# Kernel tuning notes

Hardware: AMD Instinct MI355X
Metric: run time of the kernel (lower is better)

Reference implementation:

```python
import jax, jax.numpy as jnp
import numpy as np

S = 64            # out_size
EXPAND = 1.25
FEAT_DOWN = 8
DEG2RAD = np.pi / 180.0


def setup_inputs() -> dict:
    key = jax.random.key(0)
    k1, k2, k3 = jax.random.split(key, 3)
    B, C, Hf, Wf = 2, 64, 128, 128
    N = 256
    feat = jax.random.normal(k1, (B, C, Hf, Wf), dtype=jnp.float32)
    r = jax.random.uniform(k2, (N, 5), dtype=jnp.float32)
    # values chosen so the (buggy-but-faithful) normalized-coordinate affine
    # actually samples inside the feature map (see shape_source note)
    cx = (r[:, 0] - 0.5) * 10.0
    cy = (r[:, 1] - 0.5) * 10.0
    w = 50.0 + 350.0 * r[:, 2]
    h = 50.0 + 350.0 * r[:, 3]
    deg = (r[:, 4] - 0.5) * 180.0
    obb = jnp.stack([cx, cy, w, h, deg], axis=1)
    bix = jax.random.randint(k3, (N,), 0, B)
    return {"feat": feat, "obb": obb, "bix": bix}


def _grids(obb):
    """Replicates obb_to_affine + F.affine_grid(align_corners=False).
    Returns normalized grid coords gx, gy of shape (N, S, S)."""
    scale = 1.0 / FEAT_DOWN
    cx = obb[:, 0] * scale
    cy = obb[:, 1] * scale
    ws = obb[:, 2] * scale * EXPAND
    hs = obb[:, 3] * scale * EXPAND
    th = obb[:, 4] * DEG2RAD
    c = jnp.cos(th)
    s_ = jnp.sin(th)
    sx = ws / S
    sy = hs / S
    # faithful to source: M = [[c*sx, -sin*sy, cx], [expand*sx, c*sy, cy]]
    m00 = c * sx
    m01 = -s_ * sy
    m02 = cx
    m10 = EXPAND * sx   # source uses `s` = expand here, NOT sin(theta)
    m11 = c * sy
    m12 = cy
    # affine_grid base coords (align_corners=False): (2k+1)/S - 1
    base = (2.0 * jnp.arange(S, dtype=obb.dtype) + 1.0) / S - 1.0
    x = base[None, None, :]   # output column -> x
    y = base[None, :, None]   # output row    -> y
    gx = m00[:, None, None] * x + m01[:, None, None] * y + m02[:, None, None]
    gy = m10[:, None, None] * x + m11[:, None, None] * y + m12[:, None, None]
    return gx, gy


def _rotated_roi_pool(feat, obb, bix):
    B, C, Hf, Wf = feat.shape
    gx, gy = _grids(obb)                       # (N,S,S)
    # grid_sample unnormalize (align_corners=False)
    ix = ((gx + 1.0) * Wf - 1.0) * 0.5
    iy = ((gy + 1.0) * Hf - 1.0) * 0.5
    x0f = jnp.floor(ix)
    y0f = jnp.floor(iy)
    wx1 = ix - x0f
    wy1 = iy - y0f
    x0 = x0f.astype(jnp.int32)
    y0 = y0f.astype(jnp.int32)
    b = bix[:, None, None].astype(jnp.int32)   # (N,1,1)

    def corner(yi, xi):
        valid = (xi >= 0) & (xi < Wf) & (yi >= 0) & (yi < Hf)
        yc = jnp.clip(yi, 0, Hf - 1)
        xc = jnp.clip(xi, 0, Wf - 1)
        v = feat[b, :, yc, xc]                 # (N,S,S,C) gather
        return v * valid[..., None].astype(feat.dtype)

    out = (corner(y0, x0)         * ((1.0 - wy1) * (1.0 - wx1))[..., None]
         + corner(y0, x0 + 1)     * ((1.0 - wy1) * wx1)[..., None]
         + corner(y0 + 1, x0)     * (wy1 * (1.0 - wx1))[..., None]
         + corner(y0 + 1, x0 + 1) * (wy1 * wx1)[..., None])
    return jnp.transpose(out, (0, 3, 1, 2))    # (N,C,S,S)


def reference(feat, obb, bix):
    return _rotated_roi_pool(feat, obb, bix)
```

## Files before the change

kernel.cpp:

```cpp
#include <hip/hip_runtime.h>
#include <math.h>

#define S 64
#define NC 64
#define HF 128
#define WF 128
#define HW (HF * WF)
#define SS (S * S)
#define EXPANDF 1.25f
#define FEAT_DOWN_INV 0.125f
#define DEG2RADF 0.017453292519943295f

__device__ __forceinline__ unsigned int f32_to_bf16_rne(float v) {
    unsigned int u = __float_as_uint(v);
    return (u + 0x7FFFu + ((u >> 16) & 1u)) >> 16;
}
__device__ __forceinline__ float bf16_bits_to_f32(unsigned int h) {
    return __uint_as_float(h << 16);
}

__global__ __launch_bounds__(256) void nchw_to_nhwc_bf16_kernel(
    const float*    __restrict__ feat,
    unsigned short* __restrict__ featT)
{
    __shared__ float lds[64 * 65];
    const int bh  = blockIdx.x;
    const int b   = bh >> 7;
    const int h   = bh & (HF - 1);
    const int w0  = blockIdx.y << 6;
    const int tid = threadIdx.x;
    const int t4  = tid >> 6;
    const int t64 = tid & 63;

#pragma unroll
    for (int k = 0; k < 16; ++k) {
        const int c = (k << 2) + t4;
        lds[t64 * 65 + c] = feat[(((size_t)b * NC + c) * HF + h) * WF + w0 + t64];
    }
    __syncthreads();
#pragma unroll
    for (int k = 0; k < 16; ++k) {
        const int w = (k << 2) + t4;
        featT[(((size_t)b * HF + h) * WF + w0 + w) * NC + t64] =
            (unsigned short)f32_to_bf16_rne(lds[w * 65 + t64]);
    }
}

__global__ __launch_bounds__(256) void RotatedROIPool_kernel(
    const unsigned short* __restrict__ featT,
    const float*          __restrict__ obb,
    const int*            __restrict__ bix,
    float*                __restrict__ out,
    int nwg_per_xcd)
{
    __shared__ float lds[64 * 65];

    const int bid = blockIdx.x;
    const int wg  = (bid & 7) * nwg_per_xcd + (bid >> 3);
    const int n   = wg >> 6;
    const int i   = wg & 63;

    const int tid  = threadIdx.x;
    const int wv   = tid >> 6;
    const int lane = tid & 63;
    const int s    = lane >> 3;
    const int c8   = lane & 7;

    const float o0 = obb[n * 5 + 0];
    const float o1 = obb[n * 5 + 1];
    const float o2 = obb[n * 5 + 2];
    const float o3 = obb[n * 5 + 3];
    const float o4 = obb[n * 5 + 4];

    const float cx  = o0 * FEAT_DOWN_INV;
    const float cy  = o1 * FEAT_DOWN_INV;
    const float wsc = o2 * FEAT_DOWN_INV * EXPANDF;
    const float hsc = o3 * FEAT_DOWN_INV * EXPANDF;
    const float th  = o4 * DEG2RADF;

    float sth, cth;
    sincosf(th, &sth, &cth);

    const float sx  = wsc * (1.0f / (float)S);
    const float sy  = hsc * (1.0f / (float)S);
    const float m00 = cth * sx;
    const float m01 = -sth * sy;
    const float m10 = EXPANDF * sx;
    const float m11 = cth * sy;

    const float yg = (2.0f * (float)i + 1.0f) * (1.0f / (float)S) - 1.0f;
    const float hx = m01 * yg + cx;
    const float hy = m11 * yg + cy;

    const int b = bix[n];
    const unsigned char* __restrict__ pb =
        (const unsigned char*)featT + (size_t)b * ((size_t)HW * NC * 2);

#pragma unroll
    for (int sg = 0; sg < 2; ++sg) {
        const int j = (wv << 4) + (sg << 3) + s;

        const float xg = (2.0f * (float)j + 1.0f) * (1.0f / (float)S) - 1.0f;
        const float gx = m00 * xg + hx;
        const float gy = m10 * xg + hy;

        const float ix = ((gx + 1.0f) * (float)WF - 1.0f) * 0.5f;
        const float iy = ((gy + 1.0f) * (float)HF - 1.0f) * 0.5f;

        const float x0f = floorf(ix);
        const float y0f = floorf(iy);
        const float wx1 = ix - x0f;
        const float wy1 = iy - y0f;
        const float wx0 = 1.0f - wx1;
        const float wy0 = 1.0f - wy1;

        const int x0 = (int)x0f;
        const int y0 = (int)y0f;
        const int x1 = x0 + 1;
        const int y1 = y0 + 1;

        const float vx0 = (x0 >= 0 && x0 < WF) ? 1.0f : 0.0f;
        const float vx1 = (x1 >= 0 && x1 < WF) ? 1.0f : 0.0f;
        const float vy0 = (y0 >= 0 && y0 < HF) ? 1.0f : 0.0f;
        const float vy1 = (y1 >= 0 && y1 < HF) ? 1.0f : 0.0f;

        const float w00 = wy0 * wx0 * vy0 * vx0;
        const float w01 = wy0 * wx1 * vy0 * vx1;
        const float w10 = wy1 * wx0 * vy1 * vx0;
        const float w11 = wy1 * wx1 * vy1 * vx1;

        const int x0c = min(max(x0, 0), WF - 1);
        const int x1c = min(max(x1, 0), WF - 1);
        const int y0c = min(max(y0, 0), HF - 1);
        const int y1c = min(max(y1, 0), HF - 1);

        const uint4 a00 = *((const uint4*)(pb + ((size_t)(y0c * WF + x0c) << 7)) + c8);
        const uint4 a01 = *((const uint4*)(pb + ((size_t)(y0c * WF + x1c) << 7)) + c8);
        const uint4 a10 = *((const uint4*)(pb + ((size_t)(y1c * WF + x0c) << 7)) + c8);
        const uint4 a11 = *((const uint4*)(pb + ((size_t)(y1c * WF + x1c) << 7)) + c8);

        const unsigned int* u00 = (const unsigned int*)&a00;
        const unsigned int* u01 = (const unsigned int*)&a01;
        const unsigned int* u10 = (const unsigned int*)&a10;
        const unsigned int* u11 = (const unsigned int*)&a11;

        float* L = lds + j * 65 + (c8 << 3);
#pragma unroll
        for (int m = 0; m < 4; ++m) {
            const float f00l = bf16_bits_to_f32(u00[m] & 0xFFFFu);
            const float f01l = bf16_bits_to_f32(u01[m] & 0xFFFFu);
            const float f10l = bf16_bits_to_f32(u10[m] & 0xFFFFu);
            const float f11l = bf16_bits_to_f32(u11[m] & 0xFFFFu);
            const float f00h = bf16_bits_to_f32(u00[m] >> 16);
            const float f01h = bf16_bits_to_f32(u01[m] >> 16);
            const float f10h = bf16_bits_to_f32(u10[m] >> 16);
            const float f11h = bf16_bits_to_f32(u11[m] >> 16);
            L[2 * m + 0] = w00 * f00l + w01 * f01l + w10 * f10l + w11 * f11l;
            L[2 * m + 1] = w00 * f00h + w01 * f01h + w10 * f10h + w11 * f11h;
        }
    }

    __syncthreads();

    float* __restrict__ ob = out + (size_t)n * NC * SS + (size_t)i * S;
    const int jg = tid & 15;
    const int cl = tid >> 4;
#pragma unroll
    for (int k = 0; k < 4; ++k) {
        const int c = (k << 4) + cl;
        float4 t;
        t.x = lds[(jg * 4 + 0) * 65 + c];
        t.y = lds[(jg * 4 + 1) * 65 + c];
        t.z = lds[(jg * 4 + 2) * 65 + c];
        t.w = lds[(jg * 4 + 3) * 65 + c];
        *(float4*)(ob + (size_t)c * SS + (jg << 2)) = t;
    }
}

__global__ __launch_bounds__(256) void RotatedROIPool_nchw_kernel(
    const float* __restrict__ feat, const float* __restrict__ obb,
    const int* __restrict__ bix, float* __restrict__ out)
{
    const int tid = threadIdx.x, pid = blockIdx.x;
    const int n = pid >> 4, patch = pid & 15;
    const int pi = (patch >> 2) << 4, pj = (patch & 3) << 4;
    const int w = tid >> 6, lane = tid & 63;
    const int i = pi + ((w >> 1) << 3) + (lane >> 3);
    const int j = pj + ((w & 1) << 3) + (lane & 7);
    const int c0 = blockIdx.y * 8;

    const float cx = obb[n*5+0]*FEAT_DOWN_INV, cy = obb[n*5+1]*FEAT_DOWN_INV;
    const float wsc = obb[n*5+2]*FEAT_DOWN_INV*EXPANDF, hsc = obb[n*5+3]*FEAT_DOWN_INV*EXPANDF;
    float sth, cth; sincosf(obb[n*5+4]*DEG2RADF, &sth, &cth);
    const float sx = wsc/(float)S, sy = hsc/(float)S;
    const float m00 = cth*sx, m01 = -sth*sy, m10 = EXPANDF*sx, m11 = cth*sy;
    const float xg = (2.f*j+1.f)/(float)S - 1.f, yg = (2.f*i+1.f)/(float)S - 1.f;
    const float gx = m00*xg + m01*yg + cx, gy = m10*xg + m11*yg + cy;
    const float ix = ((gx+1.f)*WF-1.f)*.5f, iy = ((gy+1.f)*HF-1.f)*.5f;
    const float x0f = floorf(ix), y0f = floorf(iy);
    const float wx1 = ix-x0f, wy1 = iy-y0f, wx0 = 1.f-wx1, wy0 = 1.f-wy1;
    const int x0 = (int)x0f, y0 = (int)y0f, x1 = x0+1, y1 = y0+1;
    const float vx0 = (x0>=0&&x0<WF)?1.f:0.f, vx1 = (x1>=0&&x1<WF)?1.f:0.f;
    const float vy0 = (y0>=0&&y0<HF)?1.f:0.f, vy1 = (y1>=0&&y1<HF)?1.f:0.f;
    const float w00 = wy0*wx0*vy0*vx0, w01 = wy0*wx1*vy0*vx1;
    const float w10 = wy1*wx0*vy1*vx0, w11 = wy1*wx1*vy1*vx1;
    const int x0c = min(max(x0,0),WF-1), x1c = min(max(x1,0),WF-1);
    const int y0c = min(max(y0,0),HF-1), y1c = min(max(y1,0),HF-1);
    const int o00 = y0c*WF+x0c, o01 = y0c*WF+x1c, o10 = y1c*WF+x0c, o11 = y1c*WF+x1c;
    const float* p = feat + (size_t)bix[n]*NC*HW + (size_t)c0*HW;
    float* op = out + (size_t)n*NC*SS + (size_t)c0*SS + (size_t)i*S + j;
#pragma unroll
    for (int g = 0; g < 2; ++g) {
        float v00[4], v01[4], v10[4], v11[4];
        const float* pc = p + (size_t)g*4*HW;
#pragma unroll
        for (int c = 0; c < 4; ++c) { v00[c]=pc[o00]; v01[c]=pc[o01]; v10[c]=pc[o10]; v11[c]=pc[o11]; pc += HW; }
        float* oc = op + (size_t)g*4*SS;
#pragma unroll
        for (int c = 0; c < 4; ++c) { *oc = w00*v00[c]+w01*v01[c]+w10*v10[c]+w11*v11[c]; oc += SS; }
    }
}

extern "C" void kernel_launch(void* const* d_in, const int* in_sizes, int n_in,
                              void* d_out, int out_size, void* d_ws, size_t ws_size,
                              hipStream_t stream) {
    const float* feat = (const float*)d_in[0];
    const float* obb  = (const float*)d_in[1];
    const int*   bx   = (const int*)d_in[2];
    float* out = (float*)d_out;

    const int N = in_sizes[1] / 5;
    const int B = in_sizes[0] / (NC * HW);
    const size_t tbytes = (size_t)B * NC * HW * sizeof(unsigned short);

    if (ws_size >= tbytes) {
        unsigned short* featT = (unsigned short*)d_ws;
        dim3 tg(B * HF, WF / 64, 1);
        nchw_to_nhwc_bf16_kernel<<<tg, 256, 0, stream>>>(feat, featT);

        const int nwg = N * S;
        RotatedROIPool_kernel<<<nwg, 256, 0, stream>>>(featT, obb, bx, out, nwg / 8);
    } else {
        dim3 grid(N * 16, NC / 8, 1);
        RotatedROIPool_nchw_kernel<<<grid, 256, 0, stream>>>(feat, obb, bx, out);
    }
}
```

Baseline: 66.63 us.

## Process four output rows per workgroup with double-buffered LDS transpose

Each workgroup now handles four consecutive output rows of one ROI instead of one. It uses two LDS buffers so the gathers for row r are issued before the transposed stores of row r-1 are written out, which overlaps gather latency with the store phase. It also amortises the per-block setup (obb load, sincos) and cuts the grid size by four. The cost is fewer workgroups (N*16), more LDS per block and higher register pressure, with launch bounds set for 4 blocks per CU.

Result: slower. 68.84 us (+3.3%).

```diff
diff --git a/kernel.cpp b/kernel.cpp
--- a/kernel.cpp
+++ b/kernel.cpp
@@ -7,6 +7,7 @@
 #define WF 128
 #define HW (HF * WF)
 #define SS (S * S)
+#define ROWS 4
 #define EXPANDF 1.25f
 #define FEAT_DOWN_INV 0.125f
 #define DEG2RADF 0.017453292519943295f
@@ -46,25 +47,27 @@
     }
 }
 
-__global__ __launch_bounds__(256) void RotatedROIPool_kernel(
+__global__ __launch_bounds__(256, 4) void RotatedROIPool_kernel(
     const unsigned short* __restrict__ featT,
     const float*          __restrict__ obb,
     const int*            __restrict__ bix,
     float*                __restrict__ out,
     int nwg_per_xcd)
 {
-    __shared__ float lds[64 * 65];
+    __shared__ float lds[2][64 * 65];
 
     const int bid = blockIdx.x;
     const int wg  = (bid & 7) * nwg_per_xcd + (bid >> 3);
-    const int n   = wg >> 6;
-    const int i   = wg & 63;
+    const int n   = wg >> 4;
+    const int i0  = (wg & 15) << 2;
 
     const int tid  = threadIdx.x;
     const int wv   = tid >> 6;
     const int lane = tid & 63;
     const int s    = lane >> 3;
     const int c8   = lane & 7;
+    const int jg   = tid & 15;
+    const int cl   = tid >> 4;
 
     const float o0 = obb[n * 5 + 0];
     const float o1 = obb[n * 5 + 1];
@@ -88,92 +91,120 @@
     const float m10 = EXPANDF * sx;
     const float m11 = cth * sy;
 
-    const float yg = (2.0f * (float)i + 1.0f) * (1.0f / (float)S) - 1.0f;
-    const float hx = m01 * yg + cx;
-    const float hy = m11 * yg + cy;
-
     const int b = bix[n];
     const unsigned char* __restrict__ pb =
         (const unsigned char*)featT + (size_t)b * ((size_t)HW * NC * 2);
 
-#pragma unroll
-    for (int sg = 0; sg < 2; ++sg) {
-        const int j = (wv << 4) + (sg << 3) + s;
-
-        const float xg = (2.0f * (float)j + 1.0f) * (1.0f / (float)S) - 1.0f;
-        const float gx = m00 * xg + hx;
-        const float gy = m10 * xg + hy;
-
-        const float ix = ((gx + 1.0f) * (float)WF - 1.0f) * 0.5f;
-        const float iy = ((gy + 1.0f) * (float)HF - 1.0f) * 0.5f;
-
-        const float x0f = floorf(ix);
-        const float y0f = floorf(iy);
-        const float wx1 = ix - x0f;
-        const float wy1 = iy - y0f;
-        const float wx0 = 1.0f - wx1;
-        const float wy0 = 1.0f - wy1;
-
-        const int x0 = (int)x0f;
-        const int y0 = (int)y0f;
-        const int x1 = x0 + 1;
-        const int y1 = y0 + 1;
-
-        const float vx0 = (x0 >= 0 && x0 < WF) ? 1.0f : 0.0f;
-        const float vx1 = (x1 >= 0 && x1 < WF) ? 1.0f : 0.0f;
-        const float vy0 = (y0 >= 0 && y0 < HF) ? 1.0f : 0.0f;
-        const float vy1 = (y1 >= 0 && y1 < HF) ? 1.0f : 0.0f;
-
-        const float w00 = wy0 * wx0 * vy0 * vx0;
-        const float w01 = wy0 * wx1 * vy0 * vx1;
-        const float w10 = wy1 * wx0 * vy1 * vx0;
-        const float w11 = wy1 * wx1 * vy1 * vx1;
-
-        const int x0c = min(max(x0, 0), WF - 1);
-        const int x1c = min(max(x1, 0), WF - 1);
-        const int y0c = min(max(y0, 0), HF - 1);
-        const int y1c = min(max(y1, 0), HF - 1);
-
-        const uint4 a00 = *((const uint4*)(pb + ((size_t)(y0c * WF + x0c) << 7)) + c8);
-        const uint4 a01 = *((const uint4*)(pb + ((size_t)(y0c * WF + x1c) << 7)) + c8);
-        const uint4 a10 = *((const uint4*)(pb + ((size_t)(y1c * WF + x0c) << 7)) + c8);
-        const uint4 a11 = *((const uint4*)(pb + ((size_t)(y1c * WF + x1c) << 7)) + c8);
-
-        const unsigned int* u00 = (const unsigned int*)&a00;
-        const unsigned int* u01 = (const unsigned int*)&a01;
-        const unsigned int* u10 = (const unsigned int*)&a10;
-        const unsigned int* u11 = (const unsigned int*)&a11;
-
-        float* L = lds + j * 65 + (c8 << 3);
-#pragma unroll
-        for (int m = 0; m < 4; ++m) {
-            const float f00l = bf16_bits_to_f32(u00[m] & 0xFFFFu);
-            const float f01l = bf16_bits_to_f32(u01[m] & 0xFFFFu);
-            const float f10l = bf16_bits_to_f32(u10[m] & 0xFFFFu);
-            const float f11l = bf16_bits_to_f32(u11[m] & 0xFFFFu);
-            const float f00h = bf16_bits_to_f32(u00[m] >> 16);
-            const float f01h = bf16_bits_to_f32(u01[m] >> 16);
-            const float f10h = bf16_bits_to_f32(u10[m] >> 16);
-            const float f11h = bf16_bits_to_f32(u11[m] >> 16);
-            L[2 * m + 0] = w00 * f00l + w01 * f01l + w10 * f10l + w11 * f11l;
-            L[2 * m + 1] = w00 * f00h + w01 * f01h + w10 * f10h + w11 * f11h;
-        }
-    }
-
-    __syncthreads();
-
-    float* __restrict__ ob = out + (size_t)n * NC * SS + (size_t)i * S;
-    const int jg = tid & 15;
-    const int cl = tid >> 4;
-#pragma unroll
-    for (int k = 0; k < 4; ++k) {
-        const int c = (k << 4) + cl;
-        float4 t;
-        t.x = lds[(jg * 4 + 0) * 65 + c];
-        t.y = lds[(jg * 4 + 1) * 65 + c];
-        t.z = lds[(jg * 4 + 2) * 65 + c];
-        t.w = lds[(jg * 4 + 3) * 65 + c];
-        *(float4*)(ob + (size_t)c * SS + (jg << 2)) = t;
+    float* __restrict__ obase = out + (size_t)n * NC * SS;
+
+#pragma unroll
+    for (int r = 0; r < ROWS; ++r) {
+        const int i = i0 + r;
+        const float yg = (2.0f * (float)i + 1.0f) * (1.0f / (float)S) - 1.0f;
+        const float hx = m01 * yg + cx;
+        const float hy = m11 * yg + cy;
+
+        uint4  a00[2], a01[2], a10[2], a11[2];
+        float  w00[2], w01[2], w10[2], w11[2];
+#pragma unroll
+        for (int sg = 0; sg < 2; ++sg) {
+            const int j = (wv << 4) + (sg << 3) + s;
+
+            const float xg = (2.0f * (float)j + 1.0f) * (1.0f / (float)S) - 1.0f;
+            const float gx = m00 * xg + hx;
+            const float gy = m10 * xg + hy;
+
+            const float ix = ((gx + 1.0f) * (float)WF - 1.0f) * 0.5f;
+            const float iy = ((gy + 1.0f) * (float)HF - 1.0f) * 0.5f;
+
+            const float x0f = floorf(ix);
+            const float y0f = floorf(iy);
+            const float wx1 = ix - x0f;
+            const float wy1 = iy - y0f;
+            const float wx0 = 1.0f - wx1;
+            const float wy0 = 1.0f - wy1;
+
+            const int x0 = (int)x0f;
+            const int y0 = (int)y0f;
+            const int x1 = x0 + 1;
+            const int y1 = y0 + 1;
+
+            const float vx0 = (x0 >= 0 && x0 < WF) ? 1.0f : 0.0f;
+            const float vx1 = (x1 >= 0 && x1 < WF) ? 1.0f : 0.0f;
+            const float vy0 = (y0 >= 0 && y0 < HF) ? 1.0f : 0.0f;
+            const float vy1 = (y1 >= 0 && y1 < HF) ? 1.0f : 0.0f;
+
+            w00[sg] = wy0 * wx0 * vy0 * vx0;
+            w01[sg] = wy0 * wx1 * vy0 * vx1;
+            w10[sg] = wy1 * wx0 * vy1 * vx0;
+            w11[sg] = wy1 * wx1 * vy1 * vx1;
+
+            const int x0c = min(max(x0, 0), WF - 1);
+            const int x1c = min(max(x1, 0), WF - 1);
+            const int y0c = min(max(y0, 0), HF - 1);
+            const int y1c = min(max(y1, 0), HF - 1);
+
+            a00[sg] = *((const uint4*)(pb + ((size_t)(y0c * WF + x0c) << 7)) + c8);
+            a01[sg] = *((const uint4*)(pb + ((size_t)(y0c * WF + x1c) << 7)) + c8);
+            a10[sg] = *((const uint4*)(pb + ((size_t)(y1c * WF + x0c) << 7)) + c8);
+            a11[sg] = *((const uint4*)(pb + ((size_t)(y1c * WF + x1c) << 7)) + c8);
+        }
+
+        if (r > 0) {
+            const float* __restrict__ Lp = lds[(r - 1) & 1];
+            float* __restrict__ ob = obase + (size_t)(i - 1) * S;
+#pragma unroll
+            for (int k = 0; k < 4; ++k) {
+                const int c = (k << 4) + cl;
+                float4 t;
+                t.x = Lp[(jg * 4 + 0) * 65 + c];
+                t.y = Lp[(jg * 4 + 1) * 65 + c];
+                t.z = Lp[(jg * 4 + 2) * 65 + c];
+                t.w = Lp[(jg * 4 + 3) * 65 + c];
+                *(float4*)(ob + (size_t)c * SS + (jg << 2)) = t;
+            }
+        }
+
+        float* __restrict__ Lc = lds[r & 1];
+#pragma unroll
+        for (int sg = 0; sg < 2; ++sg) {
+            const int j = (wv << 4) + (sg << 3) + s;
+            const unsigned int* u00 = (const unsigned int*)&a00[sg];
+            const unsigned int* u01 = (const unsigned int*)&a01[sg];
+            const unsigned int* u10 = (const unsigned int*)&a10[sg];
+            const unsigned int* u11 = (const unsigned int*)&a11[sg];
+            float* L = Lc + j * 65 + (c8 << 3);
+#pragma unroll
+            for (int m = 0; m < 4; ++m) {
+                const float f00l = bf16_bits_to_f32(u00[m] & 0xFFFFu);
+                const float f01l = bf16_bits_to_f32(u01[m] & 0xFFFFu);
+                const float f10l = bf16_bits_to_f32(u10[m] & 0xFFFFu);
+                const float f11l = bf16_bits_to_f32(u11[m] & 0xFFFFu);
+                const float f00h = bf16_bits_to_f32(u00[m] >> 16);
+                const float f01h = bf16_bits_to_f32(u01[m] >> 16);
+                const float f10h = bf16_bits_to_f32(u10[m] >> 16);
+                const float f11h = bf16_bits_to_f32(u11[m] >> 16);
+                L[2 * m + 0] = w00[sg] * f00l + w01[sg] * f01l + w10[sg] * f10l + w11[sg] * f11l;
+                L[2 * m + 1] = w00[sg] * f00h + w01[sg] * f01h + w10[sg] * f10h + w11[sg] * f11h;
+            }
+        }
+
+        __syncthreads();
+    }
+
+    {
+        const float* __restrict__ Lp = lds[(ROWS - 1) & 1];
+        float* __restrict__ ob = obase + (size_t)(i0 + ROWS - 1) * S;
+#pragma unroll
+        for (int k = 0; k < 4; ++k) {
+            const int c = (k << 4) + cl;
+            float4 t;
+            t.x = Lp[(jg * 4 + 0) * 65 + c];
+            t.y = Lp[(jg * 4 + 1) * 65 + c];
+            t.z = Lp[(jg * 4 + 2) * 65 + c];
+            t.w = Lp[(jg * 4 + 3) * 65 + c];
+            *(float4*)(ob + (size_t)c * SS + (jg << 2)) = t;
+        }
     }
 }
 
@@ -238,7 +269,7 @@
         dim3 tg(B * HF, WF / 64, 1);
         nchw_to_nhwc_bf16_kernel<<<tg, 256, 0, stream>>>(feat, featT);
 
-        const int nwg = N * S;
+        const int nwg = N * (S / ROWS);
         RotatedROIPool_kernel<<<nwg, 256, 0, stream>>>(featT, obb, bx, out, nwg / 8);
     } else {
         dim3 grid(N * 16, NC / 8, 1);
```
